# Kernel tuning notes

Hardware: AMD Instinct MI355X
Metric: run time of the kernel (lower is better)

Reference implementation:

```python
import jax, jax.numpy as jnp
import numpy as np

V = 50288; D = 768; L = 12; SPLIT = 6; L_LORA = L - SPLIT
NSTATE = 64; HDIM = 64
DIN = 2 * D                         # expand=2 -> 1536
H = DIN // HDIM                     # 24 heads
K = 4                               # depthwise conv kernel
DPROJ = 2 * DIN + 2 * NSTATE + H    # 3224
CONVD = DIN + 2 * NSTATE            # 1664
R = 8; LORA_SCALE = 2.0             # alpha/rank = 2r/r
EPS = 1e-5


def _rms(x, w):
    return x * jax.lax.rsqrt(jnp.mean(x * x, axis=-1, keepdims=True) + EPS) * w


def _ssm_scan(dt, A, Bm, Cm, xh):
    # dt:[B,T,H]  A:[H]  Bm,Cm:[B,T,N]  xh:[B,T,H,P]
    dA = jnp.exp(dt * A)
    def step(h, inp):
        dA_t, dt_t, B_t, C_t, x_t = inp
        h = dA_t[:, :, None, None] * h + (dt_t[..., None] * x_t)[..., None] * B_t[:, None, None, :]
        return h, jnp.einsum('bhpn,bn->bhp', h, C_t)
    h0 = jnp.zeros((dt.shape[0], H, HDIM, NSTATE), dt.dtype)
    xs = tuple(jnp.moveaxis(a, 1, 0) for a in (dA, dt, Bm, Cm, xh))
    _, ys = jax.lax.scan(step, h0, xs)
    return jnp.moveaxis(ys, 0, 1)  # [B,T,H,P]


@jax.checkpoint
def _mixer(u, in_w, cw, cb, dtb, A_log, Dsk, gw, out_w):
    # Mamba2 selective-scan block (ngroups=1, no biases on projections)
    Bsz, T, _ = u.shape
    zxbcdt = u @ in_w.T                              # [B,T,DPROJ]
    z = zxbcdt[..., :DIN]
    xBC = zxbcdt[..., DIN:DIN + CONVD]
    dt = zxbcdt[..., DIN + CONVD:]
    xp = jnp.pad(xBC, ((0, 0), (K - 1, 0), (0, 0)))  # causal depthwise conv1d
    xBC = jax.nn.silu(cb + sum(cw[:, k] * xp[:, k:k + T] for k in range(K)))
    xh = xBC[..., :DIN].reshape(Bsz, T, H, HDIM)
    Bm = xBC[..., DIN:DIN + NSTATE]
    Cm = xBC[..., DIN + NSTATE:]
    dt = jax.nn.softplus(dt + dtb)
    y = _ssm_scan(dt, -jnp.exp(A_log), Bm, Cm, xh) + Dsk[None, None, :, None] * xh
    y = _rms(y.reshape(Bsz, T, DIN) * jax.nn.silu(z), gw)   # gated RMSNorm
    return y @ out_w.T


def _run_base(x, res, p):
    def step(carry, q):
        x, res = carry
        res = x + res
        h = _mixer(_rms(res, q['nw']), q['iw'], q['cw'], q['cb'], q['dtb'],
                   q['al'], q['dk'], q['gw'], q['ow'])
        return (h, res), None
    (x, res), _ = jax.lax.scan(step, (x, res), p)
    return x, res


def _run_lora(x, res, p):
    def step(carry, q):
        x, res = carry
        res = x + res
        iw = q['iw'] + LORA_SCALE * (q['ibw'] @ q['iaw'])   # LoRALinear effective weight
        ow = q['ow'] + LORA_SCALE * (q['obw'] @ q['oaw'])
        h = _mixer(_rms(res, q['nw']), iw, q['cw'], q['cb'], q['dtb'],
                   q['al'], q['dk'], q['gw'], ow)
        return (h, res), None
    (x, res), _ = jax.lax.scan(step, (x, res), p)
    return x, res


def _rope(x, loop_i):
    # LoopRoPE: rotate interleaved pairs of hidden dims by angle theta_i * loop_i
    inv_freq = 1.0 / (10000.0 ** (jnp.arange(0, D, 2, dtype=jnp.float32) / D))
    f = loop_i * inv_freq
    cos_v = jnp.repeat(jnp.cos(f), 2)
    sin_v = jnp.repeat(jnp.sin(f), 2)
    x1, x2 = x[..., ::2], x[..., 1::2]
    rot = jnp.stack([-x2, x1], axis=-1).reshape(x.shape)
    return x * cos_v + rot * sin_v


def _forward(input_ids, n_loops, embedding, norm_w, in_w, conv_w, conv_b, dt_bias, A_log,
             D_skip, gnorm_w, out_w, lora_in_A, lora_in_B, lora_out_A, lora_out_B,
             core_in_w, core_conv_w, core_conv_b, core_dt_bias, core_A_log, core_D,
             core_gnorm_w, core_out_w, loop_norm_w, lifeline_gate, norm_f_w, lm_head_w):
    base = {'nw': norm_w[:SPLIT], 'iw': in_w[:SPLIT], 'cw': conv_w[:SPLIT], 'cb': conv_b[:SPLIT],
            'dtb': dt_bias[:SPLIT], 'al': A_log[:SPLIT], 'dk': D_skip[:SPLIT],
            'gw': gnorm_w[:SPLIT], 'ow': out_w[:SPLIT]}
    lora = {'nw': norm_w[SPLIT:], 'iw': in_w[SPLIT:], 'cw': conv_w[SPLIT:], 'cb': conv_b[SPLIT:],
            'dtb': dt_bias[SPLIT:], 'al': A_log[SPLIT:], 'dk': D_skip[SPLIT:],
            'gw': gnorm_w[SPLIT:], 'ow': out_w[SPLIT:],
            'iaw': lora_in_A, 'ibw': lora_in_B, 'oaw': lora_out_A, 'obw': lora_out_B}
    x = embedding[input_ids]                       # [B,T,D]
    res = jnp.zeros_like(x)                        # residual=None -> zeros
    x, res = _run_base(x, res, base)               # frozen layers [0:6]
    x, res = _run_lora(x, res, lora)               # LoRA layers [6:12]
    x_prompt = jax.lax.stop_gradient(x)            # x.clone().detach()
    for i in range(int(n_loops)):
        x = x + lifeline_gate * x_prompt           # lifeline injection
        x = _rope(x, float(i))                     # loop-index RoPE
        x, res = _run_lora(x, res, lora)           # run_lora recursion body
        x = x + _mixer(x, core_in_w, core_conv_w, core_conv_b, core_dt_bias,
                       core_A_log, core_D, core_gnorm_w, core_out_w)  # mamba2_core
        x = _rms(x, loop_norm_w)                   # loop_norm
    h = _rms(x + res, norm_f_w)                    # norm_f(x, residual, prenorm=False)
    return h @ lm_head_w.T                         # lm_head logits [B,T,V]


def setup_inputs() -> dict:
    key = jax.random.key(0)
    ks = iter(jax.random.split(key, 64))
    f32 = jnp.float32
    def w(shape, s=0.02):
        return (s * jax.random.normal(next(ks), shape)).astype(f32)
    inp = {
        'input_ids': jax.random.randint(next(ks), (2, 512), 0, 50277, dtype=jnp.int32),
        'n_loops': 3,
        'embedding': w((V, D)),
        'norm_w': jnp.ones((L, D), f32),
        'in_w': w((L, DPROJ, D)),
        'conv_w': w((L, CONVD, K), 0.2),
        'conv_b': jnp.zeros((L, CONVD), f32),
        'dt_bias': w((L, H), 0.5),
        'A_log': jnp.log(1.0 + 15.0 * jax.random.uniform(next(ks), (L, H))).astype(f32),
        'D_skip': jnp.ones((L, H), f32),
        'gnorm_w': jnp.ones((L, DIN), f32),
        'out_w': w((L, D, DIN)),
        'lora_in_A': w((L_LORA, R, D), 0.05),
        'lora_in_B': w((L_LORA, DPROJ, R), 0.05),
        'lora_out_A': w((L_LORA, R, DIN), 0.05),
        'lora_out_B': w((L_LORA, D, R), 0.05),
        'core_in_w': w((DPROJ, D)),
        'core_conv_w': w((CONVD, K), 0.2),
        'core_conv_b': jnp.zeros((CONVD,), f32),
        'core_dt_bias': w((H,), 0.5),
        'core_A_log': jnp.log(1.0 + 15.0 * jax.random.uniform(next(ks), (H,))).astype(f32),
        'core_D': jnp.ones((H,), f32),
        'core_gnorm_w': jnp.ones((DIN,), f32),
        'core_out_w': w((D, DIN)),
        'loop_norm_w': jnp.ones((D,), f32),
        'lifeline_gate': jnp.ones((D,), f32),
        'norm_f_w': jnp.ones((D,), f32),
        'lm_head_w': w((V, D)),
    }
    return inp


def reference(input_ids, n_loops, embedding, norm_w, in_w, conv_w, conv_b, dt_bias, A_log,
              D_skip, gnorm_w, out_w, lora_in_A, lora_in_B, lora_out_A, lora_out_B,
              core_in_w, core_conv_w, core_conv_b, core_dt_bias, core_A_log, core_D,
              core_gnorm_w, core_out_w, loop_norm_w, lifeline_gate, norm_f_w, lm_head_w):
    return _forward(input_ids, n_loops, embedding, norm_w, in_w, conv_w, conv_b, dt_bias,
                    A_log, D_skip, gnorm_w, out_w, lora_in_A, lora_in_B, lora_out_A,
                    lora_out_B, core_in_w, core_conv_w, core_conv_b, core_dt_bias,
                    core_A_log, core_D, core_gnorm_w, core_out_w, loop_norm_w,
                    lifeline_gate, norm_f_w, lm_head_w)
```

## Files before the change

kernel.cpp:

```cpp
#include <hip/hip_runtime.h>
#include <math.h>

constexpr int Bsz   = 2;
constexpr int Tseq  = 512;
constexpr int Mtok  = Bsz * Tseq;
constexpr int Dm    = 768;
constexpr int DINc  = 1536;
constexpr int Hn    = 24;
constexpr int NS    = 64;
constexpr int KC    = 4;
constexpr int DPROJc = 2*DINc + 2*NS + Hn;
constexpr int CONVDc = DINc + 2*NS;
constexpr int NL    = 12;
constexpr int SPL   = 6;
constexpr int LLO   = 6;
constexpr int NCH   = 8;
constexpr int Vv    = 50288;
constexpr float EPSc = 1e-5f;
constexpr int NLOOPS = 3;

#define DEVI __device__ __forceinline__

typedef _Float16 f16x8 __attribute__((ext_vector_type(8)));
typedef float    f32x4 __attribute__((ext_vector_type(4)));

DEVI float siluf(float x){ return x / (1.0f + expf(-x)); }
DEVI float softplusf(float x){ return (x > 20.0f) ? x : log1pf(expf(x)); }
DEVI unsigned short f2h(float f){
  union { _Float16 h; unsigned short u; } c;
  c.h = (_Float16)f;
  return c.u;
}
DEVI float h2f(unsigned short u){
  union { unsigned short u; _Float16 h; } c;
  c.u = u; return (float)c.h;
}

DEVI void gload16(const void* g, void* l){
  __builtin_amdgcn_global_load_lds(
      (const __attribute__((address_space(1))) void*)g,
      (__attribute__((address_space(3))) void*)l, 16, 0, 0);
}

DEVI float blk_reduce256(float v, float* sh){
  #pragma unroll
  for (int o = 32; o; o >>= 1) v += __shfl_down(v, o);
  int lane = threadIdx.x & 63, w = threadIdx.x >> 6;
  if (lane == 0) sh[w] = v;
  __syncthreads();
  return sh[0] + sh[1] + sh[2] + sh[3];
}

__global__ void k_embed(const int* __restrict__ ids, const float* __restrict__ emb,
                        float* __restrict__ x){
  int m = blockIdx.x;
  int id = ids[m];
  const float4* src = (const float4*)(emb + (size_t)id * Dm);
  float4* dst = (float4*)(x + (size_t)m * Dm);
  int i = threadIdx.x;
  dst[i] = src[i];
}

__global__ void k_f2h(const float* __restrict__ in, unsigned short* __restrict__ out, int n4){
  int e = blockIdx.x*256 + threadIdx.x;
  if (e >= n4) return;
  float4 v = ((const float4*)in)[e];
  ushort4 o; o.x=f2h(v.x); o.y=f2h(v.y); o.z=f2h(v.z); o.w=f2h(v.w);
  ((ushort4*)out)[e] = o;
}

__global__ __launch_bounds__(256) void k_addrms(const float* __restrict__ xin,
    float* __restrict__ res, unsigned short* __restrict__ ub,
    const float* __restrict__ w){
  int m = blockIdx.x, tid = threadIdx.x;
  __shared__ float sh[4];
  const float* xr = xin + (size_t)m*Dm;
  float* rr = res + (size_t)m*Dm;
  float r[3]; float ss = 0.f;
  #pragma unroll
  for (int k=0;k<3;k++){ int e = tid + k*256; float v = xr[e] + rr[e]; r[k]=v; ss += v*v; }
  ss = blk_reduce256(ss, sh);
  float rs = 1.0f / sqrtf(ss/(float)Dm + EPSc);
  #pragma unroll
  for (int k=0;k<3;k++){
    int e = tid + k*256;
    rr[e] = r[k];
    ub[(size_t)m*Dm+e] = f2h(r[k]*rs*w[e]);
  }
}

__global__ __launch_bounds__(256) void k_addrms_p(const float* __restrict__ part,
    float* __restrict__ res, unsigned short* __restrict__ ub,
    const float* __restrict__ w){
  int m = blockIdx.x, tid = threadIdx.x;
  __shared__ float sh[4];
  const size_t tot = (size_t)Mtok*Dm;
  float* rr = res + (size_t)m*Dm;
  float r[3]; float ss = 0.f;
  #pragma unroll
  for (int k=0;k<3;k++){
    int e = tid + k*256;
    size_t idx = (size_t)m*Dm + e;
    float v = rr[e] + part[idx] + part[tot+idx] + part[2*tot+idx] + part[3*tot+idx];
    r[k]=v; ss += v*v;
  }
  ss = blk_reduce256(ss, sh);
  float rs = 1.0f / sqrtf(ss/(float)Dm + EPSc);
  #pragma unroll
  for (int k=0;k<3;k++){
    int e = tid + k*256;
    rr[e] = r[k];
    ub[(size_t)m*Dm+e] = f2h(r[k]*rs*w[e]);
  }
}

__global__ void k_sum_xp(const float* __restrict__ part, float* __restrict__ x,
                         float* __restrict__ xp){
  size_t e = (size_t)blockIdx.x*256 + threadIdx.x;
  const size_t tot = (size_t)Mtok*Dm;
  if (e >= tot) return;
  float v = part[e] + part[tot+e] + part[2*tot+e] + part[3*tot+e];
  x[e] = v; xp[e] = v;
}

__global__ void k_f2h_sum(const float* __restrict__ part, float* __restrict__ x,
                          unsigned short* __restrict__ ub){
  size_t e = (size_t)blockIdx.x*256 + threadIdx.x;
  const size_t tot = (size_t)Mtok*Dm;
  if (e >= tot) return;
  float v = part[e] + part[tot+e] + part[2*tot+e] + part[3*tot+e];
  x[e] = v; ub[e] = f2h(v);
}

__global__ __launch_bounds__(256) void k_rms_p(const float* __restrict__ part,
    float* __restrict__ x, const float* __restrict__ w){
  int m = blockIdx.x, tid = threadIdx.x;
  __shared__ float sh[4];
  const size_t tot = (size_t)Mtok*Dm;
  float* xr = x + (size_t)m*Dm;
  float r[3]; float ss = 0.f;
  #pragma unroll
  for (int k=0;k<3;k++){
    int e = tid + k*256;
    size_t idx = (size_t)m*Dm + e;
    float v = xr[e] + part[idx] + part[tot+idx] + part[2*tot+idx] + part[3*tot+idx];
    r[k]=v; ss += v*v;
  }
  ss = blk_reduce256(ss, sh);
  float rs = 1.0f / sqrtf(ss/(float)Dm + EPSc);
  #pragma unroll
  for (int k=0;k<3;k++){ int e = tid + k*256; xr[e] = r[k]*rs*w[e]; }
}

__global__ __launch_bounds__(128) void k_liferope(float* __restrict__ x,
    const float* __restrict__ xp, const float* __restrict__ gate, float iF){
  int m = blockIdx.x, tid = threadIdx.x;
  float* xr = x + (size_t)m*Dm;
  const float* pr = xp + (size_t)m*Dm;
  #pragma unroll
  for (int k=0;k<3;k++){
    int j = tid + k*128;
    int d0 = 2*j, d1 = d0+1;
    float v0 = xr[d0] + gate[d0]*pr[d0];
    float v1 = xr[d1] + gate[d1]*pr[d1];
    float invf = expf(-9.210340371976184f * ((float)(2*j) * (1.0f/768.0f)));
    float f = iF * invf;
    float cv = cosf(f), sv = sinf(f);
    xr[d0] = v0*cv - v1*sv;
    xr[d1] = v1*cv + v0*sv;
  }
}

__global__ __launch_bounds__(256) void k_gemm_h(
    const unsigned short* __restrict__ A,
    const unsigned short* __restrict__ Bw,
    void* __restrict__ Cv, int Nd, int Kd, int outmode){
  __shared__ __align__(16) char smem[65536];
  unsigned short (*lA)[128*64] = (unsigned short (*)[128*64])smem;
  unsigned short (*lB)[128*64] = (unsigned short (*)[128*64])(smem + 32768);
  const int tid  = threadIdx.x;
  const int lane = tid & 63;
  const int wv   = tid >> 6;
  const int wm   = wv >> 1, wn = wv & 1;
  const int gx = gridDim.x, gy = gridDim.y;
  const int nwg = gx*gy;
  const int flat = blockIdx.x + gx*blockIdx.y;
  const int q = nwg >> 3, r = nwg & 7;
  const int xcd = flat & 7, pos = flat >> 3;
  const int lg = (xcd < r ? xcd*(q+1) : r*(q+1) + (xcd - r)*q) + pos;
  const int m_idx = lg % gy, n_idx = lg / gy;
  const int n0 = n_idx * 128;
  const int m0 = m_idx * 128;
  const int KS = gridDim.z;
  const int kchunk = Kd / KS;
  const int kbeg = blockIdx.z * kchunk;
  const int nsteps = kchunk / 64;

  f32x4 acc[4][4] = {};

  auto stage = [&](int buf, int k0){
    #pragma unroll
    for (int i=0;i<4;i++){
      int seg = tid + i*256;
      int row = seg >> 3;
      int c8  = (seg & 7) ^ (row & 7);
      gload16(A + (size_t)(m0 + row)*Kd + k0 + c8*8, &lA[buf][seg*8]);
      int rn = n0 + row; rn = (rn < Nd) ? rn : (Nd - 1);
      gload16(Bw + (size_t)rn*Kd + k0 + c8*8, &lB[buf][seg*8]);
    }
  };

  stage(0, kbeg);
  for (int t=0; t<nsteps; ++t){
    const int cur = t & 1;
    if (t+1 < nsteps){
      stage(cur^1, kbeg + (t+1)*64);
      __builtin_amdgcn_sched_barrier(0);
      asm volatile("s_waitcnt vmcnt(8)" ::: "memory");
    } else {
      asm volatile("s_waitcnt vmcnt(0)" ::: "memory");
    }
    __builtin_amdgcn_s_barrier();
    __builtin_amdgcn_sched_barrier(0);
    #pragma unroll
    for (int kk=0; kk<2; kk++){
      f16x8 af[4], bfr[4];
      #pragma unroll
      for (int f=0; f<4; f++){
        int rowa = wm*64 + f*16 + (lane & 15);
        int ba = rowa*128 + ((kk*64 + (lane>>4)*16) ^ ((rowa & 7) << 4));
        af[f] = *(const f16x8*)((const char*)&lA[cur][0] + ba);
        int rowb = wn*64 + f*16 + (lane & 15);
        int bb = rowb*128 + ((kk*64 + (lane>>4)*16) ^ ((rowb & 7) << 4));
        bfr[f] = *(const f16x8*)((const char*)&lB[cur][0] + bb);
      }
      #pragma unroll
      for (int fm=0; fm<4; fm++)
        #pragma unroll
        for (int fn=0; fn<4; fn++)
          acc[fm][fn] = __builtin_amdgcn_mfma_f32_16x16x32_f16(af[fm], bfr[fn], acc[fm][fn], 0, 0, 0);
    }
    __builtin_amdgcn_s_barrier();
  }

  float (*eps)[132] = (float (*)[132])smem;
  #pragma unroll
  for (int half = 0; half < 2; ++half){
    __syncthreads();
    if (wm == half){
      #pragma unroll
      for (int fm=0; fm<4; fm++)
        #pragma unroll
        for (int fn=0; fn<4; fn++)
          #pragma unroll
          for (int rr=0; rr<4; rr++){
            int rloc = fm*16 + ((lane>>4)<<2) + rr;
            int ncol = wn*64 + fn*16 + (lane & 15);
            eps[rloc][ncol] = acc[fm][fn][rr];
          }
    }
    __syncthreads();
    #pragma unroll
    for (int i=0;i<8;i++){
      int idx = tid + i*256;
      int row = idx >> 5, c4 = idx & 31;
      int n = n0 + c4*4;
      if (n < Nd){
        float4 v4 = *(const float4*)&eps[row][c4*4];
        int m = m0 + half*64 + row;
        if (outmode == 0){
          float* Cb = (float*)Cv + (size_t)blockIdx.z*((size_t)Mtok*Nd);
          *(float4*)&Cb[(size_t)m*Nd + n] = v4;
        } else if (outmode == 1){
          *(float4*)&((float*)Cv)[(size_t)m*Nd + n] = v4;
        } else {
          ushort4 o; o.x=f2h(v4.x); o.y=f2h(v4.y); o.z=f2h(v4.z); o.w=f2h(v4.w);
          *(ushort4*)&((unsigned short*)Cv)[(size_t)m*Nd + n] = o;
        }
      }
    }
  }
}

__global__ void k_prep_in(const float* __restrict__ W12, const float* __restrict__ Wc,
    const float* __restrict__ lA, const float* __restrict__ lB,
    unsigned short* __restrict__ out){
  const int tot4 = DPROJc*Dm/4;
  int e4 = blockIdx.x*256 + threadIdx.x;
  if (e4 >= tot4) return;
  int l = blockIdx.y;
  const float* W = (l < 12) ? W12 + (size_t)l*DPROJc*Dm : Wc;
  const int k4n = Dm/4;
  int n = e4 / k4n, k4 = e4 - n*k4n;
  float4 wv = *(const float4*)(W + (size_t)n*Dm + k4*4);
  float s0=wv.x, s1=wv.y, s2=wv.z, s3=wv.w;
  if (l >= SPL && l < 12){
    int ll = l - SPL;
    const float* Bl = lB + (size_t)ll*DPROJc*8;
    const float* Al = lA + (size_t)ll*8*Dm;
    #pragma unroll
    for (int r=0;r<8;r++){
      float b = 2.0f * Bl[n*8+r];
      float4 a = *(const float4*)(Al + (size_t)r*Dm + k4*4);
      s0 += b*a.x; s1 += b*a.y; s2 += b*a.z; s3 += b*a.w;
    }
  }
  ushort4 o; o.x=f2h(s0); o.y=f2h(s1); o.z=f2h(s2); o.w=f2h(s3);
  ((ushort4*)(out + (size_t)l*DPROJc*Dm))[e4] = o;
}

__global__ void k_prep_out(const float* __restrict__ W12, const float* __restrict__ Wc,
    const float* __restrict__ lA, const float* __restrict__ lB,
    unsigned short* __restrict__ out){
  const int tot4 = Dm*DINc/4;
  int e4 = blockIdx.x*256 + threadIdx.x;
  if (e4 >= tot4) return;
  int l = blockIdx.y;
  const float* W = (l < 12) ? W12 + (size_t)l*Dm*DINc : Wc;
  const int k4n = DINc/4;
  int n = e4 / k4n, k4 = e4 - n*k4n;
  float4 wv = *(const float4*)(W + (size_t)n*DINc + k4*4);
  float s0=wv.x, s1=wv.y, s2=wv.z, s3=wv.w;
  if (l >= SPL && l < 12){
    int ll = l - SPL;
    const float* Bl = lB + (size_t)ll*Dm*8;
    const float* Al = lA + (size_t)ll*8*DINc;
    #pragma unroll
    for (int r=0;r<8;r++){
      float b = 2.0f * Bl[n*8+r];
      float4 a = *(const float4*)(Al + (size_t)r*DINc + k4*4);
      s0 += b*a.x; s1 += b*a.y; s2 += b*a.z; s3 += b*a.w;
    }
  }
  ushort4 o; o.x=f2h(s0); o.y=f2h(s1); o.z=f2h(s2); o.w=f2h(s3);
  ((ushort4*)(out + (size_t)l*Dm*DINc))[e4] = o;
}

DEVI f16x8 ldfrag(const unsigned short (*T)[72], int row, int k0){
  return *(const f16x8*)&T[row][k0];
}

__global__ __launch_bounds__(256) void k_s1(const unsigned short* __restrict__ zxh,
    const float* __restrict__ cw, const float* __restrict__ cb,
    const float* __restrict__ dtb, const float* __restrict__ alog,
    float* __restrict__ S, float* __restrict__ ctot){
  int bh = blockIdx.x; int b = bh / Hn, h = bh % Hn; int c = blockIdx.y;
  __shared__ unsigned short XT[64][72];
  __shared__ unsigned short BwT[64][72];
  __shared__ float wv[64];
  int tid = threadIdx.x;
  int base_m = b*Tseq + c*64;
  if (tid < 64){
    float Av = -expf(alog[h]);
    float zdt = h2f(zxh[(size_t)(base_m+tid)*DPROJc + DINc + CONVDc + h]) + dtb[h];
    float dt = softplusf(zdt);
    float s = dt * Av;
    #pragma unroll
    for (int o=1;o<64;o<<=1){ float v = __shfl_up(s, o); if (tid >= o) s += v; }
    if (tid == 63) ctot[bh*NCH + c] = s;
    float ce = __shfl(s, 63);
    wv[tid] = expf(ce - s) * dt;
  }
  __syncthreads();
  int ch = tid & 63;
  int t0 = (tid >> 6) * 16;
  int tl = c*64 + t0;
  {
    int cc = h*64 + ch;
    float4 w4 = *(const float4*)&cw[cc*KC];
    float bias = cb[cc];
    const unsigned short* zp = zxh + (size_t)base_m*DPROJc + DINc + cc;
    float v0 = (tl >= 3) ? h2f(zp[(long)(t0-3)*DPROJc]) : 0.f;
    float v1 = (tl >= 2) ? h2f(zp[(long)(t0-2)*DPROJc]) : 0.f;
    float v2 = (tl >= 1) ? h2f(zp[(long)(t0-1)*DPROJc]) : 0.f;
    #pragma unroll
    for (int i=0;i<16;i++){
      float v3 = h2f(zp[(long)(t0+i)*DPROJc]);
      float o = bias + w4.x*v0 + w4.y*v1 + w4.z*v2 + w4.w*v3;
      XT[ch][t0+i] = f2h(siluf(o));
      v0=v1; v1=v2; v2=v3;
    }
  }
  {
    int cc = DINc + ch;
    float4 w4 = *(const float4*)&cw[cc*KC];
    float bias = cb[cc];
    const unsigned short* zp = zxh + (size_t)base_m*DPROJc + DINc + cc;
    float v0 = (tl >= 3) ? h2f(zp[(long)(t0-3)*DPROJc]) : 0.f;
    float v1 = (tl >= 2) ? h2f(zp[(long)(t0-2)*DPROJc]) : 0.f;
    float v2 = (tl >= 1) ? h2f(zp[(long)(t0-1)*DPROJc]) : 0.f;
    #pragma unroll
    for (int i=0;i<16;i++){
      float v3 = h2f(zp[(long)(t0+i)*DPROJc]);
      float o = bias + w4.x*v0 + w4.y*v1 + w4.z*v2 + w4.w*v3;
      BwT[ch][t0+i] = f2h(siluf(o) * wv[t0+i]);
      v0=v1; v1=v2; v2=v3;
    }
  }
  __syncthreads();
  int lane = tid & 63, wid = tid >> 6, wmp = wid >> 1, wnn = wid & 1;
  f32x4 acc[2][2] = {};
  #pragma unroll
  for (int kk=0; kk<2; kk++){
    int k0 = kk*32 + (lane>>4)*8;
    f16x8 a[2], bf[2];
    #pragma unroll
    for (int f=0; f<2; f++){
      a[f]  = ldfrag(XT,  wmp*32 + f*16 + (lane&15), k0);
      bf[f] = ldfrag(BwT, wnn*32 + f*16 + (lane&15), k0);
    }
    #pragma unroll
    for (int fm=0; fm<2; fm++)
      #pragma unroll
      for (int fn=0; fn<2; fn++)
        acc[fm][fn] = __builtin_amdgcn_mfma_f32_16x16x32_f16(a[fm], bf[fn], acc[fm][fn], 0, 0, 0);
  }
  float* Sb = S + ((size_t)(bh*NCH + c))*4096;
  #pragma unroll
  for (int fm=0; fm<2; fm++)
    #pragma unroll
    for (int fn=0; fn<2; fn++)
      #pragma unroll
      for (int rg=0; rg<4; rg++){
        int p = wmp*32 + fm*16 + ((lane>>4)<<2) + rg;
        int n = wnn*32 + fn*16 + (lane&15);
        Sb[p*64 + n] = acc[fm][fn][rg];
      }
}

__global__ __launch_bounds__(256) void k_s3(const unsigned short* __restrict__ zxh,
    const float* __restrict__ cw, const float* __restrict__ cb,
    const float* __restrict__ dtb, const float* __restrict__ alog,
    const float* __restrict__ Sg, const float* __restrict__ ctot,
    const float* __restrict__ Dsk, unsigned short* __restrict__ y){
  int bh = blockIdx.x; int b = bh / Hn, h = bh % Hn; int c = blockIdx.y;
  __shared__ unsigned short Ch[64][72];
  __shared__ unsigned short Bh[64][72];
  __shared__ unsigned short XhT[64][72];
  __shared__ unsigned short hT[64][72];
  __shared__ unsigned short Mh[64][72];
  __shared__ float cumS[64], dtS[64];
  __shared__ float wch[NCH];
  int tid = threadIdx.x;
  int base_m = b*Tseq + c*64;
  if (tid < 64){
    float Av = -expf(alog[h]);
    float zdt = h2f(zxh[(size_t)(base_m+tid)*DPROJc + DINc + CONVDc + h]) + dtb[h];
    float dt = softplusf(zdt);
    float s = dt * Av;
    #pragma unroll
    for (int o=1;o<64;o<<=1){ float v = __shfl_up(s, o); if (tid >= o) s += v; }
    cumS[tid] = s;
    dtS[tid]  = dt;
  }
  if (tid >= 64 && tid < 64 + NCH){
    int cp = tid - 64;
    float s = 0.f;
    for (int j = cp+1; j < c; ++j) s += ctot[bh*NCH + j];
    wch[cp] = (cp < c) ? expf(s) : 0.f;
  }
  int ch = tid & 63;
  int t0 = (tid >> 6) * 16;
  int tl = c*64 + t0;
  {
    int cc = h*64 + ch;
    float4 w4 = *(const float4*)&cw[cc*KC];
    float bias = cb[cc];
    const unsigned short* zp = zxh + (size_t)base_m*DPROJc + DINc + cc;
    float v0 = (tl >= 3) ? h2f(zp[(long)(t0-3)*DPROJc]) : 0.f;
    float v1 = (tl >= 2) ? h2f(zp[(long)(t0-2)*DPROJc]) : 0.f;
    float v2 = (tl >= 1) ? h2f(zp[(long)(t0-1)*DPROJc]) : 0.f;
    #pragma unroll
    for (int i=0;i<16;i++){
      float v3 = h2f(zp[(long)(t0+i)*DPROJc]);
      float o = bias + w4.x*v0 + w4.y*v1 + w4.z*v2 + w4.w*v3;
      XhT[ch][t0+i] = f2h(siluf(o));
      v0=v1; v1=v2; v2=v3;
    }
  }
  {
    int cc = DINc + ch;
    float4 w4 = *(const float4*)&cw[cc*KC];
    float bias = cb[cc];
    const unsigned short* zp = zxh + (size_t)base_m*DPROJc + DINc + cc;
    float v0 = (tl >= 3) ? h2f(zp[(long)(t0-3)*DPROJc]) : 0.f;
    float v1 = (tl >= 2) ? h2f(zp[(long)(t0-2)*DPROJc]) : 0.f;
    float v2 = (tl >= 1) ? h2f(zp[(long)(t0-1)*DPROJc]) : 0.f;
    #pragma unroll
    for (int i=0;i<16;i++){
      float v3 = h2f(zp[(long)(t0+i)*DPROJc]);
      float o = bias + w4.x*v0 + w4.y*v1 + w4.z*v2 + w4.w*v3;
      Bh[t0+i][ch] = f2h(siluf(o));
      v0=v1; v1=v2; v2=v3;
    }
  }
  {
    int cc = DINc + NS + ch;
    float4 w4 = *(const float4*)&cw[cc*KC];
    float bias = cb[cc];
    const unsigned short* zp = zxh + (size_t)base_m*DPROJc + DINc + cc;
    float v0 = (tl >= 3) ? h2f(zp[(long)(t0-3)*DPROJc]) : 0.f;
    float v1 = (tl >= 2) ? h2f(zp[(long)(t0-2)*DPROJc]) : 0.f;
    float v2 = (tl >= 1) ? h2f(zp[(long)(t0-1)*DPROJc]) : 0.f;
    #pragma unroll
    for (int i=0;i<16;i++){
      float v3 = h2f(zp[(long)(t0+i)*DPROJc]);
      float o = bias + w4.x*v0 + w4.y*v1 + w4.z*v2 + w4.w*v3;
      Ch[t0+i][ch] = f2h(siluf(o));
      v0=v1; v1=v2; v2=v3;
    }
  }
  __syncthreads();
  int lane = tid & 63, wid = tid >> 6, wmt = wid >> 1, wns = wid & 1;
  f32x4 g[2][2] = {};
  #pragma unroll
  for (int kk=0; kk<2; kk++){
    int k0 = kk*32 + (lane>>4)*8;
    f16x8 a[2], bf[2];
    #pragma unroll
    for (int f=0; f<2; f++){
      a[f]  = ldfrag(Ch, wmt*32 + f*16 + (lane&15), k0);
      bf[f] = ldfrag(Bh, wns*32 + f*16 + (lane&15), k0);
    }
    #pragma unroll
    for (int fm=0; fm<2; fm++)
      #pragma unroll
      for (int fn=0; fn<2; fn++)
        g[fm][fn] = __builtin_amdgcn_mfma_f32_16x16x32_f16(a[fm], bf[fn], g[fm][fn], 0, 0, 0);
  }
  #pragma unroll
  for (int fm=0; fm<2; fm++)
    #pragma unroll
    for (int fn=0; fn<2; fn++)
      #pragma unroll
      for (int rg=0; rg<4; rg++){
        int t = wmt*32 + fm*16 + ((lane>>4)<<2) + rg;
        int s = wns*32 + fn*16 + (lane&15);
        float val = (s <= t) ? expf(cumS[t] - cumS[s]) * dtS[s] * g[fm][fn][rg] : 0.f;
        Mh[t][s] = f2h(val);
      }
  {
    const float* Sb0 = Sg + ((size_t)bh*NCH)*4096;
    for (int e4 = tid; e4 < 1024; e4 += 256){
      float a0=0.f, a1=0.f, a2=0.f, a3=0.f;
      for (int cp = 0; cp < c; ++cp){
        float wv = wch[cp];
        float4 sv = ((const float4*)(Sb0 + (size_t)cp*4096))[e4];
        a0 += wv*sv.x; a1 += wv*sv.y; a2 += wv*sv.z; a3 += wv*sv.w;
      }
      int p = (e4 << 2) >> 6, n = (e4 << 2) & 63;
      ushort4 o; o.x=f2h(a0); o.y=f2h(a1); o.z=f2h(a2); o.w=f2h(a3);
      *(ushort4*)&hT[p][n] = o;
    }
  }
  __syncthreads();
  f32x4 aL[2][2] = {}, aS[2][2] = {};
  #pragma unroll
  for (int kk=0; kk<2; kk++){
    int k0 = kk*32 + (lane>>4)*8;
    f16x8 m_[2], x_[2], c_[2], h_[2];
    #pragma unroll
    for (int f=0; f<2; f++){
      m_[f] = ldfrag(Mh,  wmt*32 + f*16 + (lane&15), k0);
      x_[f] = ldfrag(XhT, wns*32 + f*16 + (lane&15), k0);
      c_[f] = ldfrag(Ch,  wmt*32 + f*16 + (lane&15), k0);
      h_[f] = ldfrag(hT,  wns*32 + f*16 + (lane&15), k0);
    }
    #pragma unroll
    for (int fm=0; fm<2; fm++)
      #pragma unroll
      for (int fn=0; fn<2; fn++){
        aL[fm][fn] = __builtin_amdgcn_mfma_f32_16x16x32_f16(m_[fm], x_[fn], aL[fm][fn], 0, 0, 0);
        aS[fm][fn] = __builtin_amdgcn_mfma_f32_16x16x32_f16(c_[fm], h_[fn], aS[fm][fn], 0, 0, 0);
      }
  }
  float Dh = Dsk[h];
  #pragma unroll
  for (int fm=0; fm<2; fm++)
    #pragma unroll
    for (int fn=0; fn<2; fn++)
      #pragma unroll
      for (int rg=0; rg<4; rg++){
        int t = wmt*32 + fm*16 + ((lane>>4)<<2) + rg;
        int p = wns*32 + fn*16 + (lane&15);
        float Pt = expf(cumS[t]);
        float xv = h2f(XhT[p][t]);
        float o = aL[fm][fn][rg] + Pt*aS[fm][fn][rg] + Dh*xv;
        y[(size_t)(base_m+t)*DINc + h*64 + p] = f2h(o);
      }
}

__global__ __launch_bounds__(256) void k_gate(const unsigned short* __restrict__ zxh,
    const unsigned short* __restrict__ y, unsigned short* __restrict__ yb,
    const float* __restrict__ gw){
  int m = blockIdx.x, tid = threadIdx.x;
  __shared__ float sh[4];
  const unsigned short* zr = zxh + (size_t)m*DPROJc;
  const unsigned short* yr = y + (size_t)m*DINc;
  float g[6]; float ss = 0.f;
  #pragma unroll
  for (int k=0;k<6;k++){
    int e = tid + k*256;
    float z = h2f(zr[e]);
    float v = h2f(yr[e]) * siluf(z);
    g[k] = v; ss += v*v;
  }
  ss = blk_reduce256(ss, sh);
  float rs = 1.0f / sqrtf(ss/(float)DINc + EPSc);
  #pragma unroll
  for (int k=0;k<6;k++){
    int e = tid + k*256;
    yb[(size_t)m*DINc + e] = f2h(g[k]*rs*gw[e]);
  }
}

struct WSP {
  float *x,*res,*xp,*ctot,*Sc,*part;
  unsigned short *zxh,*yh,*ub,*yb,*wib,*wob,*whb;
};

static void run_mixer_h(hipStream_t st, const WSP& w, const unsigned short* ub_in,
    const unsigned short* iw, const float* cw, const float* cb, const float* dtb,
    const float* al, const float* dk, const float* gw, const unsigned short* ow){
  dim3 gIn((DPROJc + 127)/128, Mtok/128, 1);
  k_gemm_h<<<gIn, 256, 0, st>>>(ub_in, iw, w.zxh, DPROJc, Dm, 2);
  k_s1<<<dim3(Bsz*Hn, NCH), 256, 0, st>>>(w.zxh, cw, cb, dtb, al, w.Sc, w.ctot);
  k_s3<<<dim3(Bsz*Hn, NCH), 256, 0, st>>>(w.zxh, cw, cb, dtb, al, w.Sc, w.ctot,
                                           dk, w.yh);
  k_gate<<<Mtok, 256, 0, st>>>(w.zxh, w.yh, w.yb, gw);
  dim3 gOut(Dm/128, Mtok/128, 4);
  k_gemm_h<<<gOut, 256, 0, st>>>(w.yb, ow, w.part, Dm, DINc, 0);
}

extern "C" void kernel_launch(void* const* d_in, const int* in_sizes, int n_in,
                              void* d_out, int out_size, void* d_ws, size_t ws_size,
                              hipStream_t stream){
  const int*   ids        = (const int*)  d_in[0];
  const float* emb        = (const float*)d_in[2];
  const float* norm_w     = (const float*)d_in[3];
  const float* in_w       = (const float*)d_in[4];
  const float* conv_w     = (const float*)d_in[5];
  const float* conv_b     = (const float*)d_in[6];
  const float* dt_bias    = (const float*)d_in[7];
  const float* A_log      = (const float*)d_in[8];
  const float* D_skip     = (const float*)d_in[9];
  const float* gnorm_w    = (const float*)d_in[10];
  const float* out_w      = (const float*)d_in[11];
  const float* lora_in_A  = (const float*)d_in[12];
  const float* lora_in_B  = (const float*)d_in[13];
  const float* lora_out_A = (const float*)d_in[14];
  const float* lora_out_B = (const float*)d_in[15];
  const float* core_in_w  = (const float*)d_in[16];
  const float* core_conv_w= (const float*)d_in[17];
  const float* core_conv_b= (const float*)d_in[18];
  const float* core_dtb   = (const float*)d_in[19];
  const float* core_A_log = (const float*)d_in[20];
  const float* core_D     = (const float*)d_in[21];
  const float* core_gw    = (const float*)d_in[22];
  const float* core_out_w = (const float*)d_in[23];
  const float* loop_norm_w= (const float*)d_in[24];
  const float* life_gate  = (const float*)d_in[25];
  const float* norm_f_w   = (const float*)d_in[26];
  const float* lm_head_w  = (const float*)d_in[27];
  (void)in_sizes; (void)n_in; (void)out_size; (void)ws_size;

  char* pb = (char*)d_ws;
  auto balloc = [&](size_t bytes){
    char* q = pb; pb += (bytes + 255) & ~(size_t)255; return q;
  };
  WSP w;
  w.x    = (float*)balloc((size_t)Mtok*Dm*4);
  w.res  = (float*)balloc((size_t)Mtok*Dm*4);
  w.xp   = (float*)balloc((size_t)Mtok*Dm*4);
  w.ctot = (float*)balloc((size_t)Bsz*Hn*NCH*4);
  w.Sc   = (float*)balloc((size_t)Bsz*Hn*NCH*4096*4);
  w.part = (float*)balloc((size_t)4*Mtok*Dm*4);
  w.zxh  = (unsigned short*)balloc((size_t)Mtok*DPROJc*2);
  w.yh   = (unsigned short*)balloc((size_t)Mtok*DINc*2);
  w.ub   = (unsigned short*)balloc((size_t)Mtok*Dm*2);
  w.yb   = (unsigned short*)balloc((size_t)Mtok*DINc*2);

  const size_t IWN = (size_t)DPROJc*Dm;
  const size_t OWN = (size_t)Dm*DINc;
  const size_t HWN = (size_t)Vv*Dm;
  w.wib = (unsigned short*)balloc(13*IWN*2);
  w.wob = (unsigned short*)balloc(13*OWN*2);
  w.whb = (unsigned short*)balloc(HWN*2);

  k_prep_in<<<dim3((IWN/4 + 255)/256, 13), 256, 0, stream>>>(
      in_w, core_in_w, lora_in_A, lora_in_B, w.wib);
  k_prep_out<<<dim3((OWN/4 + 255)/256, 13), 256, 0, stream>>>(
      out_w, core_out_w, lora_out_A, lora_out_B, w.wob);
  k_f2h<<<(HWN/4 + 255)/256, 256, 0, stream>>>(lm_head_w, w.whb, (int)(HWN/4));

  k_embed<<<Mtok, 192, 0, stream>>>(ids, emb, w.x);
  hipMemsetAsync(w.res, 0, (size_t)Mtok*Dm*sizeof(float), stream);

  const size_t totMD = (size_t)Mtok*Dm;

  auto mixer_l = [&](int l){
    run_mixer_h(stream, w, w.ub,
        w.wib + (size_t)l*IWN, conv_w + (size_t)l*CONVDc*KC, conv_b + (size_t)l*CONVDc,
        dt_bias + (size_t)l*Hn, A_log + (size_t)l*Hn, D_skip + (size_t)l*Hn,
        gnorm_w + (size_t)l*DINc, w.wob + (size_t)l*OWN);
  };
  k_addrms<<<Mtok, 256, 0, stream>>>(w.x, w.res, w.ub, norm_w);
  mixer_l(0);
  for (int l=1; l<NL; l++){
    k_addrms_p<<<Mtok, 256, 0, stream>>>(w.part, w.res, w.ub, norm_w + (size_t)l*Dm);
    mixer_l(l);
  }
  k_sum_xp<<<(totMD + 255)/256, 256, 0, stream>>>(w.part, w.x, w.xp);
  for (int i=0;i<NLOOPS;i++){
    k_liferope<<<Mtok, 128, 0, stream>>>(w.x, w.xp, life_gate, (float)i);
    k_addrms<<<Mtok, 256, 0, stream>>>(w.x, w.res, w.ub, norm_w + (size_t)SPL*Dm);
    mixer_l(SPL);
    for (int l=SPL+1; l<NL; l++){
      k_addrms_p<<<Mtok, 256, 0, stream>>>(w.part, w.res, w.ub, norm_w + (size_t)l*Dm);
      mixer_l(l);
    }
    k_f2h_sum<<<(totMD + 255)/256, 256, 0, stream>>>(w.part, w.x, w.ub);
    run_mixer_h(stream, w, w.ub,
        w.wib + 12*IWN, core_conv_w, core_conv_b, core_dtb, core_A_log, core_D,
        core_gw, w.wob + 12*OWN);
    k_rms_p<<<Mtok, 256, 0, stream>>>(w.part, w.x, loop_norm_w);
  }
  k_addrms<<<Mtok, 256, 0, stream>>>(w.x, w.res, w.ub, norm_f_w);
  dim3 gHead((Vv + 127)/128, Mtok/128, 1);
  k_gemm_h<<<gHead, 256, 0, stream>>>(w.ub, w.whb, d_out, Vv, Dm, 1);
}
```

Baseline: 2.271 ms.

## Fuse gated RMSNorm into scan output and out-proj GEMM epilogue

Removes the separate gating/RMSNorm kernel. The scan-output kernel now applies the SiLU(z) gate and writes per-head partial sums of squares. The norm weight is folded into the out-projection weights during prep, and the out-proj GEMM epilogue applies the per-row rsqrt scale computed from those partial sums. This saves one launch and a full read/write pass over the y buffer per mixer, at the cost of extra shared memory and z loads in the scan kernel. Applying the row scale after the split-K partial accumulation is valid because the scale is linear per row.

Measured after the change: 2.329 ms. 1.03x slower.

```diff
diff --git a/kernel.cpp b/kernel.cpp
--- a/kernel.cpp
+++ b/kernel.cpp
@@ -174,7 +174,8 @@
 __global__ __launch_bounds__(256) void k_gemm_h(
     const unsigned short* __restrict__ A,
     const unsigned short* __restrict__ Bw,
-    void* __restrict__ Cv, int Nd, int Kd, int outmode){
+    void* __restrict__ Cv, int Nd, int Kd, int outmode,
+    const float* __restrict__ psum){
   __shared__ __align__(16) char smem[65536];
   unsigned short (*lA)[128*64] = (unsigned short (*)[128*64])smem;
   unsigned short (*lB)[128*64] = (unsigned short (*)[128*64])(smem + 32768);
@@ -243,6 +244,15 @@
     __builtin_amdgcn_s_barrier();
   }
 
+  float* lRs = (float*)(smem + 40960);
+  if (psum && tid < 128){
+    const float* pr = psum + (size_t)(m0 + tid)*Hn;
+    float s = 0.f;
+    #pragma unroll
+    for (int hh=0; hh<Hn; hh++) s += pr[hh];
+    lRs[tid] = 1.0f / sqrtf(s*(1.0f/(float)DINc) + EPSc);
+  }
+
   float (*eps)[132] = (float (*)[132])smem;
   #pragma unroll
   for (int half = 0; half < 2; ++half){
@@ -267,6 +277,10 @@
       int n = n0 + c4*4;
       if (n < Nd){
         float4 v4 = *(const float4*)&eps[row][c4*4];
+        if (psum){
+          float rs = lRs[half*64 + row];
+          v4.x *= rs; v4.y *= rs; v4.z *= rs; v4.w *= rs;
+        }
         int m = m0 + half*64 + row;
         if (outmode == 0){
           float* Cb = (float*)Cv + (size_t)blockIdx.z*((size_t)Mtok*Nd);
@@ -311,12 +325,14 @@
 
 __global__ void k_prep_out(const float* __restrict__ W12, const float* __restrict__ Wc,
     const float* __restrict__ lA, const float* __restrict__ lB,
+    const float* __restrict__ gnw, const float* __restrict__ core_gw,
     unsigned short* __restrict__ out){
   const int tot4 = Dm*DINc/4;
   int e4 = blockIdx.x*256 + threadIdx.x;
   if (e4 >= tot4) return;
   int l = blockIdx.y;
   const float* W = (l < 12) ? W12 + (size_t)l*Dm*DINc : Wc;
+  const float* gw = (l < 12) ? gnw + (size_t)l*DINc : core_gw;
   const int k4n = DINc/4;
   int n = e4 / k4n, k4 = e4 - n*k4n;
   float4 wv = *(const float4*)(W + (size_t)n*DINc + k4*4);
@@ -332,6 +348,8 @@
       s0 += b*a.x; s1 += b*a.y; s2 += b*a.z; s3 += b*a.w;
     }
   }
+  float4 g4 = *(const float4*)(gw + k4*4);
+  s0 *= g4.x; s1 *= g4.y; s2 *= g4.z; s3 *= g4.w;
   ushort4 o; o.x=f2h(s0); o.y=f2h(s1); o.z=f2h(s2); o.w=f2h(s3);
   ((ushort4*)(out + (size_t)l*Dm*DINc))[e4] = o;
 }
@@ -432,15 +450,18 @@
     const float* __restrict__ cw, const float* __restrict__ cb,
     const float* __restrict__ dtb, const float* __restrict__ alog,
     const float* __restrict__ Sg, const float* __restrict__ ctot,
-    const float* __restrict__ Dsk, unsigned short* __restrict__ y){
+    const float* __restrict__ Dsk, unsigned short* __restrict__ g_out,
+    float* __restrict__ psum){
   int bh = blockIdx.x; int b = bh / Hn, h = bh % Hn; int c = blockIdx.y;
   __shared__ unsigned short Ch[64][72];
   __shared__ unsigned short Bh[64][72];
   __shared__ unsigned short XhT[64][72];
   __shared__ unsigned short hT[64][72];
   __shared__ unsigned short Mh[64][72];
+  __shared__ unsigned short zh[64][72];
   __shared__ float cumS[64], dtS[64];
   __shared__ float wch[NCH];
+  __shared__ float sqS[64][2];
   int tid = threadIdx.x;
   int base_m = b*Tseq + c*64;
   if (tid < 64){
@@ -458,6 +479,11 @@
     float s = 0.f;
     for (int j = cp+1; j < c; ++j) s += ctot[bh*NCH + j];
     wch[cp] = (cp < c) ? expf(s) : 0.f;
+  }
+  for (int e4 = tid; e4 < 1024; e4 += 256){
+    int row = e4 >> 4, c4 = e4 & 15;
+    *(ushort4*)&zh[row][c4*4] =
+        *(const ushort4*)(zxh + (size_t)(base_m+row)*DPROJc + h*64 + c4*4);
   }
   int ch = tid & 63;
   int t0 = (tid >> 6) * 16;
@@ -576,60 +602,46 @@
   }
   float Dh = Dsk[h];
   #pragma unroll
-  for (int fm=0; fm<2; fm++)
-    #pragma unroll
-    for (int fn=0; fn<2; fn++)
-      #pragma unroll
-      for (int rg=0; rg<4; rg++){
-        int t = wmt*32 + fm*16 + ((lane>>4)<<2) + rg;
+  for (int fm=0; fm<2; fm++){
+    #pragma unroll
+    for (int rg=0; rg<4; rg++){
+      int t = wmt*32 + fm*16 + ((lane>>4)<<2) + rg;
+      float Pt = expf(cumS[t]);
+      float sq = 0.f;
+      #pragma unroll
+      for (int fn=0; fn<2; fn++){
         int p = wns*32 + fn*16 + (lane&15);
-        float Pt = expf(cumS[t]);
         float xv = h2f(XhT[p][t]);
-        float o = aL[fm][fn][rg] + Pt*aS[fm][fn][rg] + Dh*xv;
-        y[(size_t)(base_m+t)*DINc + h*64 + p] = f2h(o);
+        float yv = aL[fm][fn][rg] + Pt*aS[fm][fn][rg] + Dh*xv;
+        float z = h2f(zh[t][p]);
+        float gv = yv * siluf(z);
+        g_out[(size_t)(base_m+t)*DINc + h*64 + p] = f2h(gv);
+        sq += gv*gv;
       }
-}
-
-__global__ __launch_bounds__(256) void k_gate(const unsigned short* __restrict__ zxh,
-    const unsigned short* __restrict__ y, unsigned short* __restrict__ yb,
-    const float* __restrict__ gw){
-  int m = blockIdx.x, tid = threadIdx.x;
-  __shared__ float sh[4];
-  const unsigned short* zr = zxh + (size_t)m*DPROJc;
-  const unsigned short* yr = y + (size_t)m*DINc;
-  float g[6]; float ss = 0.f;
-  #pragma unroll
-  for (int k=0;k<6;k++){
-    int e = tid + k*256;
-    float z = h2f(zr[e]);
-    float v = h2f(yr[e]) * siluf(z);
-    g[k] = v; ss += v*v;
-  }
-  ss = blk_reduce256(ss, sh);
-  float rs = 1.0f / sqrtf(ss/(float)DINc + EPSc);
-  #pragma unroll
-  for (int k=0;k<6;k++){
-    int e = tid + k*256;
-    yb[(size_t)m*DINc + e] = f2h(g[k]*rs*gw[e]);
-  }
+      sq += __shfl_xor(sq, 1); sq += __shfl_xor(sq, 2);
+      sq += __shfl_xor(sq, 4); sq += __shfl_xor(sq, 8);
+      if ((lane & 15) == 0) sqS[t][wns] = sq;
+    }
+  }
+  __syncthreads();
+  if (tid < 64) psum[(size_t)(base_m + tid)*Hn + h] = sqS[tid][0] + sqS[tid][1];
 }
 
 struct WSP {
-  float *x,*res,*xp,*ctot,*Sc,*part;
-  unsigned short *zxh,*yh,*ub,*yb,*wib,*wob,*whb;
+  float *x,*res,*xp,*ctot,*Sc,*part,*psum;
+  unsigned short *zxh,*ub,*yb,*wib,*wob,*whb;
 };
 
 static void run_mixer_h(hipStream_t st, const WSP& w, const unsigned short* ub_in,
     const unsigned short* iw, const float* cw, const float* cb, const float* dtb,
-    const float* al, const float* dk, const float* gw, const unsigned short* ow){
+    const float* al, const float* dk, const unsigned short* ow){
   dim3 gIn((DPROJc + 127)/128, Mtok/128, 1);
-  k_gemm_h<<<gIn, 256, 0, st>>>(ub_in, iw, w.zxh, DPROJc, Dm, 2);
+  k_gemm_h<<<gIn, 256, 0, st>>>(ub_in, iw, w.zxh, DPROJc, Dm, 2, nullptr);
   k_s1<<<dim3(Bsz*Hn, NCH), 256, 0, st>>>(w.zxh, cw, cb, dtb, al, w.Sc, w.ctot);
   k_s3<<<dim3(Bsz*Hn, NCH), 256, 0, st>>>(w.zxh, cw, cb, dtb, al, w.Sc, w.ctot,
-                                           dk, w.yh);
-  k_gate<<<Mtok, 256, 0, st>>>(w.zxh, w.yh, w.yb, gw);
+                                           dk, w.yb, w.psum);
   dim3 gOut(Dm/128, Mtok/128, 4);
-  k_gemm_h<<<gOut, 256, 0, st>>>(w.yb, ow, w.part, Dm, DINc, 0);
+  k_gemm_h<<<gOut, 256, 0, st>>>(w.yb, ow, w.part, Dm, DINc, 0, w.psum);
 }
 
 extern "C" void kernel_launch(void* const* d_in, const int* in_sizes, int n_in,
@@ -675,8 +687,8 @@
   w.ctot = (float*)balloc((size_t)Bsz*Hn*NCH*4);
   w.Sc   = (float*)balloc((size_t)Bsz*Hn*NCH*4096*4);
   w.part = (float*)balloc((size_t)4*Mtok*Dm*4);
+  w.psum = (float*)balloc((size_t)Mtok*Hn*4);
   w.zxh  = (unsigned short*)balloc((size_t)Mtok*DPROJc*2);
-  w.yh   = (unsigned short*)balloc((size_t)Mtok*DINc*2);
   w.ub   = (unsigned short*)balloc((size_t)Mtok*Dm*2);
   w.yb   = (unsigned short*)balloc((size_t)Mtok*DINc*2);
 
@@ -690,7 +702,7 @@
   k_prep_in<<<dim3((IWN/4 + 255)/256, 13), 256, 0, stream>>>(
       in_w, core_in_w, lora_in_A, lora_in_B, w.wib);
   k_prep_out<<<dim3((OWN/4 + 255)/256, 13), 256, 0, stream>>>(
-      out_w, core_out_w, lora_out_A, lora_out_B, w.wob);
+      out_w, core_out_w, lora_out_A, lora_out_B, gnorm_w, core_gw, w.wob);
   k_f2h<<<(HWN/4 + 255)/256, 256, 0, stream>>>(lm_head_w, w.whb, (int)(HWN/4));
 
   k_embed<<<Mtok, 192, 0, stream>>>(ids, emb, w.x);
@@ -702,7 +714,7 @@
     run_mixer_h(stream, w, w.ub,
         w.wib + (size_t)l*IWN, conv_w + (size_t)l*CONVDc*KC, conv_b + (size_t)l*CONVDc,
         dt_bias + (size_t)l*Hn, A_log + (size_t)l*Hn, D_skip + (size_t)l*Hn,
-        gnorm_w + (size_t)l*DINc, w.wob + (size_t)l*OWN);
+        w.wob + (size_t)l*OWN);
   };
   k_addrms<<<Mtok, 256, 0, stream>>>(w.x, w.res, w.ub, norm_w);
   mixer_l(0);
@@ -722,10 +734,10 @@
     k_f2h_sum<<<(totMD + 255)/256, 256, 0, stream>>>(w.part, w.x, w.ub);
     run_mixer_h(stream, w, w.ub,
         w.wib + 12*IWN, core_conv_w, core_conv_b, core_dtb, core_A_log, core_D,
-        core_gw, w.wob + 12*OWN);
+        w.wob + 12*OWN);
     k_rms_p<<<Mtok, 256, 0, stream>>>(w.part, w.x, loop_norm_w);
   }
   k_addrms<<<Mtok, 256, 0, stream>>>(w.x, w.res, w.ub, norm_f_w);
   dim3 gHead((Vv + 127)/128, Mtok/128, 1);
-  k_gemm_h<<<gHead, 256, 0, stream>>>(w.ub, w.whb, d_out, Vv, Dm, 1);
-}
+  k_gemm_h<<<gHead, 256, 0, stream>>>(w.ub, w.whb, d_out, Vv, Dm, 1, nullptr);
+}
```
